# Kernel optimization log

Measured on AMD Instinct MI355X. Metric: run time of the kernel, lower is better.

The kernel has to match this reference:

```python
import jax, jax.numpy as jnp
import numpy as np

N, E, G = 50000, 600000, 512      # nodes, edges, graphs
FX, FE, H, OUT = 6, 4, 128, 1     # node feat, edge feat, hidden, output
T = 1.0                           # GENConv softmax temperature (learn_t=False default)
EPS = 1e-7                        # GENConv message eps


def setup_inputs() -> dict:
    key = jax.random.key(0)
    ks = jax.random.split(key, 12)
    return {
        "x": jax.random.normal(ks[0], (N, FX), jnp.float32),
        "edge_attr": jax.random.normal(ks[1], (E, FE), jnp.float32),
        "edge_index": jax.random.randint(ks[2], (2, E), 0, N),
        "batch": jnp.sort(jax.random.randint(ks[3], (N,), 0, G)),
        # node / edge encoders
        "wn": jax.random.normal(ks[4], (FX, H), jnp.float32) / np.sqrt(FX),
        "bn": jnp.zeros((H,), jnp.float32),
        "we": jax.random.normal(ks[5], (FE, H), jnp.float32) / np.sqrt(FE),
        "be": jnp.zeros((H,), jnp.float32),
        # 3 GENConv layers, params stacked on leading axis
        "cw1": jax.random.normal(ks[6], (3, H, 2 * H), jnp.float32) / np.sqrt(H),
        "cb1": jnp.zeros((3, 2 * H), jnp.float32),
        "cg": jnp.ones((3, 2 * H), jnp.float32),   # batchnorm gamma
        "cbt": jnp.zeros((3, 2 * H), jnp.float32), # batchnorm beta
        "cw2": jax.random.normal(ks[7], (3, 2 * H, H), jnp.float32) / np.sqrt(2 * H),
        "cb2": jnp.zeros((3, H), jnp.float32),
        # final dense
        "wd": jax.random.normal(ks[8], (H, OUT), jnp.float32) / np.sqrt(H),
        "bd": jnp.zeros((OUT,), jnp.float32),
    }


def _gen_conv(x, src, dst, edge_attr, w1, b1, g, bt, w2, b2):
    # message: relu(x_j + e_ij) + eps, aggregated with scatter-softmax over dst
    m = jax.nn.relu(x[src] + edge_attr) + EPS               # [E, H]
    z = m * T
    zmax = jax.lax.stop_gradient(jax.ops.segment_max(z, dst, num_segments=N))
    ez = jnp.exp(z - zmax[dst])
    denom = jax.ops.segment_sum(ez, dst, num_segments=N)
    alpha = ez / (denom[dst] + 1e-16)
    aggr = jax.ops.segment_sum(m * alpha, dst, num_segments=N)  # [N, H]
    h = aggr + x                                             # residual input to MLP
    # MLP: Linear(H,2H) -> BatchNorm(train mode) -> ReLU -> Linear(2H,H)
    h1 = h @ w1 + b1
    mu = h1.mean(0)
    var = h1.var(0)
    h1 = (h1 - mu) * jax.lax.rsqrt(var + 1e-5) * g + bt
    return jax.nn.relu(h1) @ w2 + b2


def reference(x, edge_attr, edge_index, batch, wn, bn, we, be,
              cw1, cb1, cg, cbt, cw2, cb2, wd, bd):
    src, dst = edge_index[0], edge_index[1]
    h = x @ wn + bn            # node encoder
    ea = edge_attr @ we + be   # edge encoder (shared across the 3 convs)
    for i in range(3):
        h = jax.nn.relu(_gen_conv(h, src, dst, ea,
                                  cw1[i], cb1[i], cg[i], cbt[i], cw2[i], cb2[i]))
    # global mean pool over graphs
    s = jax.ops.segment_sum(h, batch, num_segments=G)
    cnt = jax.ops.segment_sum(jnp.ones((N,), h.dtype), batch, num_segments=G)
    pooled = s / jnp.maximum(cnt, 1.0)[:, None]              # [G, H]
    return jax.nn.sigmoid(pooled @ wd + bd)                  # [G, OUT]
```

## Files before the change

kernel.cpp:

```cpp
#include <hip/hip_runtime.h>
#include <hip/hip_fp16.h>


#define HH 128
#define H2 256
#define MMP 256

typedef __attribute__((ext_vector_type(8))) short short8v;
typedef __attribute__((ext_vector_type(4))) float f32x4;
typedef __attribute__((ext_vector_type(2))) float f32x2;

__device__ __forceinline__ short f2bf(float f) {
  union { float f; unsigned u; } v; v.f = f;
  unsigned r = v.u + 0x7fff + ((v.u >> 16) & 1);
  return (short)(r >> 16);
}
__device__ __forceinline__ float bf2f(ushort s) {
  union { unsigned u; float f; } v; v.u = ((unsigned)s) << 16;
  return v.f;
}
__device__ __forceinline__ f32x2 splat2(float s) { return (f32x2){s, s}; }

__global__ void k_encode(const float* __restrict__ x, const float* __restrict__ wn,
                         const float* __restrict__ bnb, __half* __restrict__ h16, int n) {
  int c = threadIdx.x & 127;
  int node = blockIdx.x * 2 + (threadIdx.x >> 7);
  if (node >= n) return;
  const float* xr = x + (size_t)node * 6;
  float acc = bnb[c];
#pragma unroll
  for (int k = 0; k < 6; ++k) acc = fmaf(xr[k], wn[k * HH + c], acc);
  h16[(size_t)node * HH + c] = __float2half(acc);
}

__global__ void k_hist(const int* __restrict__ dst, int* __restrict__ counts,
                       const int* __restrict__ batch, float* __restrict__ cntf,
                       int E, int N) {
  int e = blockIdx.x * 256 + threadIdx.x;
  if (e < E) atomicAdd(&counts[dst[e]], 1);
  if (e < N) atomicAdd(&cntf[batch[e]], 1.f);
}

__global__ void k_scan(const int* __restrict__ counts, int* __restrict__ rowptr, int n) {
  __shared__ int wsum[16];
  __shared__ int carry;
  int t = threadIdx.x;
  int lane = t & 63, w = t >> 6;
  if (t == 0) carry = 0;
  __syncthreads();
  for (int base = 0; base < n; base += 4096) {
    int idx = base + t * 4;
    int4 v = make_int4(0, 0, 0, 0);
    if (idx + 3 < n) {
      v = *(const int4*)(counts + idx);
    } else {
      if (idx < n)     v.x = counts[idx];
      if (idx + 1 < n) v.y = counts[idx + 1];
      if (idx + 2 < n) v.z = counts[idx + 2];
    }
    int tsum = v.x + v.y + v.z + v.w;
    int x = tsum;
#pragma unroll
    for (int d = 1; d < 64; d <<= 1) {
      int y = __shfl_up(x, d);
      if (lane >= d) x += y;
    }
    if (lane == 63) wsum[w] = x;
    __syncthreads();
    if (w == 0 && lane < 16) {
      int s = wsum[lane];
#pragma unroll
      for (int d = 1; d < 16; d <<= 1) {
        int y = __shfl_up(s, d);
        if (lane >= d) s += y;
      }
      wsum[lane] = s;
    }
    __syncthreads();
    int waveoff = (w == 0) ? 0 : wsum[w - 1];
    int c0 = carry;
    int excl = c0 + waveoff + x - tsum;
    int4 o;
    o.x = excl;
    o.y = excl + v.x;
    o.z = o.y + v.y;
    o.w = o.z + v.z;
    if (idx + 3 < n) {
      *(int4*)(rowptr + idx) = o;
    } else {
      if (idx < n)     rowptr[idx] = o.x;
      if (idx + 1 < n) rowptr[idx + 1] = o.y;
      if (idx + 2 < n) rowptr[idx + 2] = o.z;
    }
    __syncthreads();
    if (t == 0) carry = c0 + wsum[15];
    __syncthreads();
  }
  if (t == 0) rowptr[n] = carry;
}

__global__ void k_fill(const int* __restrict__ src, const int* __restrict__ dst,
                       const float4* __restrict__ eattr,
                       const int* __restrict__ rowptr, int* __restrict__ fill,
                       int* __restrict__ ssrc, float4* __restrict__ eattrs, int E) {
  int e = blockIdx.x * 256 + threadIdx.x;
  if (e >= E) return;
  int d = dst[e];
  int pos = rowptr[d] + atomicAdd(&fill[d], 1);
  ssrc[pos] = src[e];
  eattrs[pos] = eattr[e];
}

__global__ __launch_bounds__(256) void k_conv(
    const __half* __restrict__ h16, const float4* __restrict__ eattrs,
    const float* __restrict__ we, const float* __restrict__ be,
    const int* __restrict__ rowptr, const int* __restrict__ ssrc,
    ushort* __restrict__ hresb, int n) {
  int d = blockIdx.x * 4 + (threadIdx.x >> 6);
  if (d >= n) return;
  int lane = threadIdx.x & 63;
  int c0 = lane * 2;
  f32x2 W0 = *(const f32x2*)(we + c0);
  f32x2 W1 = *(const f32x2*)(we + 128 + c0);
  f32x2 W2 = *(const f32x2*)(we + 256 + c0);
  f32x2 W3 = *(const f32x2*)(we + 384 + c0);
  f32x2 BE = *(const f32x2*)(be + c0);
  const f32x2 ZERO = splat2(0.f);
  const f32x2 EPS = splat2(1e-7f);
  int p0 = rowptr[d], p1 = rowptr[d + 1];
  f32x2 Sab = ZERO, Wab = ZERO, Scd = ZERO, Wcd = ZERO;
  int p = p0;
  for (; p + 4 <= p1; p += 4) {
    int sA = ssrc[p], sB = ssrc[p + 1], sC = ssrc[p + 2], sD = ssrc[p + 3];
    float4 aA = eattrs[p], aB = eattrs[p + 1], aC = eattrs[p + 2], aD = eattrs[p + 3];
    __half2 hA2 = *(const __half2*)(h16 + (size_t)sA * HH + c0);
    __half2 hB2 = *(const __half2*)(h16 + (size_t)sB * HH + c0);
    __half2 hC2 = *(const __half2*)(h16 + (size_t)sC * HH + c0);
    __half2 hD2 = *(const __half2*)(h16 + (size_t)sD * HH + c0);
    float2 hA = __half22float2(hA2), hB = __half22float2(hB2);
    float2 hC = __half22float2(hC2), hD = __half22float2(hD2);
    f32x2 eA = W0 * splat2(aA.x) + (W1 * splat2(aA.y) + (W2 * splat2(aA.z) + (W3 * splat2(aA.w) + BE)));
    f32x2 eB = W0 * splat2(aB.x) + (W1 * splat2(aB.y) + (W2 * splat2(aB.z) + (W3 * splat2(aB.w) + BE)));
    f32x2 eC = W0 * splat2(aC.x) + (W1 * splat2(aC.y) + (W2 * splat2(aC.z) + (W3 * splat2(aC.w) + BE)));
    f32x2 eD = W0 * splat2(aD.x) + (W1 * splat2(aD.y) + (W2 * splat2(aD.z) + (W3 * splat2(aD.w) + BE)));
    f32x2 mA = __builtin_elementwise_max((f32x2){hA.x, hA.y} + eA, ZERO) + EPS;
    f32x2 mB = __builtin_elementwise_max((f32x2){hB.x, hB.y} + eB, ZERO) + EPS;
    f32x2 mC = __builtin_elementwise_max((f32x2){hC.x, hC.y} + eC, ZERO) + EPS;
    f32x2 mD = __builtin_elementwise_max((f32x2){hD.x, hD.y} + eD, ZERO) + EPS;
    f32x2 xA = (f32x2){__expf(mA.x), __expf(mA.y)};
    f32x2 xB = (f32x2){__expf(mB.x), __expf(mB.y)};
    f32x2 xC = (f32x2){__expf(mC.x), __expf(mC.y)};
    f32x2 xD = (f32x2){__expf(mD.x), __expf(mD.y)};
    Sab += xA + xB;
    Scd += xC + xD;
    Wab += mA * xA + mB * xB;
    Wcd += mC * xC + mD * xD;
  }
  for (; p < p1; ++p) {
    int s = ssrc[p];
    float4 a = eattrs[p];
    __half2 hv2 = *(const __half2*)(h16 + (size_t)s * HH + c0);
    float2 hv = __half22float2(hv2);
    f32x2 e = W0 * splat2(a.x) + (W1 * splat2(a.y) + (W2 * splat2(a.z) + (W3 * splat2(a.w) + BE)));
    f32x2 m = __builtin_elementwise_max((f32x2){hv.x, hv.y} + e, ZERO) + EPS;
    f32x2 xe = (f32x2){__expf(m.x), __expf(m.y)};
    Sab += xe;
    Wab += m * xe;
  }
  f32x2 S = Sab + Scd, W = Wab + Wcd;
  __half2 hd2 = *(const __half2*)(h16 + (size_t)d * HH + c0);
  float2 hd = __half22float2(hd2);
  float r0 = W.x / (S.x + 1e-16f) + hd.x;
  float r1 = W.y / (S.y + 1e-16f) + hd.y;
  ushort2 o;
  o.x = (ushort)f2bf(r0);
  o.y = (ushort)f2bf(r1);
  *(ushort2*)(hresb + (size_t)d * HH + c0) = o;
}

__global__ void k_wconv(const float* __restrict__ W, short* __restrict__ out,
                        int logn, int K) {
  int layer = blockIdx.y;
  int total = K << logn;
  int e = blockIdx.x * 256 + threadIdx.x;
  if (e >= total) return;
  const float* Wl = W + (size_t)layer * total;
  short* ol = out + (size_t)layer * total;
  int k = e >> logn, col = e & ((1 << logn) - 1);
  int ty = col >> 7, colL = col & 127;
  int wc = colL >> 6, n = (colL >> 4) & 3, l15 = colL & 15;
  int kc = k >> 7, kl = k & 127;
  int ksl = kl >> 5, lhi = (kl >> 3) & 3, j = kl & 7;
  int KC = K >> 7;
  size_t idx = (size_t)(ty * KC + kc) * 16384 +
               ((((wc * 4 + n) * 4 + ksl) * 64 + lhi * 16 + l15) * 8 + j);
  ol[idx] = f2bf(Wl[e]);
}

__global__ __launch_bounds__(256) void k_mm1p(
    const ushort* __restrict__ Ab, const short* __restrict__ Bf,
    const float* __restrict__ bias, ushort* __restrict__ Cb,
    float* __restrict__ partial, int M, int mtiles) {
  __shared__ float red[256];
  int t = threadIdx.x;
  int bx = blockIdx.x, ty = blockIdx.y;
  int lane = t & 63, w = t >> 6;
  int wr = w >> 1, wc = w & 1;
  int l15 = lane & 15, lhi = lane >> 4;
  const short* Bt = Bf + (size_t)ty * 16384;
  short8v breg[4][4];
#pragma unroll
  for (int n = 0; n < 4; ++n)
#pragma unroll
    for (int ksl = 0; ksl < 4; ++ksl)
      breg[n][ksl] = *(const short8v*)(Bt + ((((wc * 4 + n) * 4 + ksl) * 64 + lane) * 8));
  float bb[4];
#pragma unroll
  for (int n = 0; n < 4; ++n) bb[n] = bias[ty * 128 + wc * 64 + n * 16 + l15];
  float cs[4] = {0.f, 0.f, 0.f, 0.f}, cq[4] = {0.f, 0.f, 0.f, 0.f};

  short8v a_cur[2][4], a_nxt[2][4];
  int tile = bx;
  if (tile < mtiles) {
    int row0 = tile * 64;
#pragma unroll
    for (int m = 0; m < 2; ++m) {
      int grow = row0 + (wr * 2 + m) * 16 + l15;
      if (grow < M) {
        const ushort* ap = Ab + (size_t)grow * HH + lhi * 8;
#pragma unroll
        for (int ksl = 0; ksl < 4; ++ksl) a_cur[m][ksl] = *(const short8v*)(ap + ksl * 32);
      } else {
#pragma unroll
        for (int ksl = 0; ksl < 4; ++ksl) a_cur[m][ksl] = (short8v){0,0,0,0,0,0,0,0};
      }
    }
  }
#pragma unroll 1
  for (; tile < mtiles; tile += MMP) {
    int nt = tile + MMP;
    if (nt < mtiles) {
      int row0n = nt * 64;
#pragma unroll
      for (int m = 0; m < 2; ++m) {
        int grow = row0n + (wr * 2 + m) * 16 + l15;
        if (grow < M) {
          const ushort* ap = Ab + (size_t)grow * HH + lhi * 8;
#pragma unroll
          for (int ksl = 0; ksl < 4; ++ksl) a_nxt[m][ksl] = *(const short8v*)(ap + ksl * 32);
        } else {
#pragma unroll
          for (int ksl = 0; ksl < 4; ++ksl) a_nxt[m][ksl] = (short8v){0,0,0,0,0,0,0,0};
        }
      }
    }
    f32x4 acc[2][4];
#pragma unroll
    for (int m = 0; m < 2; ++m)
#pragma unroll
      for (int n = 0; n < 4; ++n) acc[m][n] = (f32x4){0.f, 0.f, 0.f, 0.f};
#pragma unroll
    for (int ksl = 0; ksl < 4; ++ksl)
#pragma unroll
      for (int m = 0; m < 2; ++m)
#pragma unroll
        for (int n = 0; n < 4; ++n)
          acc[m][n] = __builtin_amdgcn_mfma_f32_16x16x32_bf16(a_cur[m][ksl], breg[n][ksl],
                                                              acc[m][n], 0, 0, 0);
    int row0 = tile * 64;
#pragma unroll
    for (int n = 0; n < 4; ++n) {
      int colL = wc * 64 + n * 16 + l15;
#pragma unroll
      for (int m = 0; m < 2; ++m) {
        int rbase = row0 + wr * 32 + m * 16 + lhi * 4;
#pragma unroll
        for (int r = 0; r < 4; ++r) {
          int row = rbase + r;
          if (row < M) {
            float o = acc[m][n][r] + bb[n];
            Cb[(size_t)row * H2 + ty * 128 + colL] = (ushort)f2bf(o);
            cs[n] += o; cq[n] += o * o;
          }
        }
      }
    }
#pragma unroll
    for (int m = 0; m < 2; ++m)
#pragma unroll
      for (int ksl = 0; ksl < 4; ++ksl) a_cur[m][ksl] = a_nxt[m][ksl];
  }
  red[t] = 0.f;
  __syncthreads();
#pragma unroll
  for (int n = 0; n < 4; ++n) {
    int colL = wc * 64 + n * 16 + l15;
    atomicAdd(&red[colL], cs[n]);
    atomicAdd(&red[128 + colL], cq[n]);
  }
  __syncthreads();
  partial[((size_t)(ty * MMP + bx)) * 256 + t] = red[t];
}

__global__ __launch_bounds__(1024) void k_bnfin(
    const float* __restrict__ partial, const float* __restrict__ g,
    const float* __restrict__ bt, float* __restrict__ scale,
    float* __restrict__ shift, float invN) {
  __shared__ float shs[1024], shq[1024];
  int t = threadIdx.x;
  int c = t & 255, seg = t >> 8;
  int ty = c >> 7, cl = c & 127;
  float s = 0.f, q = 0.f;
  const float* base = partial + (size_t)ty * MMP * 256;
#pragma unroll 8
  for (int bx = seg * 64; bx < seg * 64 + 64; ++bx) {
    s += base[(size_t)bx * 256 + cl];
    q += base[(size_t)bx * 256 + 128 + cl];
  }
  shs[t] = s; shq[t] = q;
  __syncthreads();
  if (t < 256) {
    s = shs[t] + shs[t + 256] + shs[t + 512] + shs[t + 768];
    q = shq[t] + shq[t + 256] + shq[t + 512] + shq[t + 768];
    float mu = s * invN;
    float var = q * invN - mu * mu;
    float rs = rsqrtf(var + 1e-5f);
    float sc = rs * g[t];
    scale[t] = sc;
    shift[t] = bt[t] - mu * sc;
  }
}

__global__ __launch_bounds__(256) void k_mm2f(
    const ushort* __restrict__ Ab, const short* __restrict__ Bf,
    const float* __restrict__ bias, const float* __restrict__ scale,
    const float* __restrict__ shift, __half* __restrict__ h16, int M) {
  int t = threadIdx.x;
  int row0 = blockIdx.x * 64;
  int lane = t & 63, w = t >> 6;
  int wr = w >> 1, wc = w & 1;
  int l15 = lane & 15, lhi = lane >> 4;
  int grow[2]; bool gv[2];
#pragma unroll
  for (int m = 0; m < 2; ++m) {
    grow[m] = row0 + (wr * 2 + m) * 16 + l15;
    gv[m] = grow[m] < M;
  }
  f32x4 acc[2][4];
#pragma unroll
  for (int m = 0; m < 2; ++m)
#pragma unroll
    for (int n = 0; n < 4; ++n) acc[m][n] = (f32x4){0.f, 0.f, 0.f, 0.f};
#pragma unroll 1
  for (int kc = 0; kc < 2; ++kc) {
    const short* Bk = Bf + (size_t)kc * 16384;
    short8v breg[4][4];
#pragma unroll
    for (int n = 0; n < 4; ++n)
#pragma unroll
      for (int ksl = 0; ksl < 4; ++ksl)
        breg[n][ksl] = *(const short8v*)(Bk + ((((wc * 4 + n) * 4 + ksl) * 64 + lane) * 8));
#pragma unroll
    for (int ksl = 0; ksl < 4; ++ksl) {
      int kb = kc * 128 + (ksl * 4 + lhi) * 8;
      float4 sc0 = *(const float4*)(scale + kb);
      float4 sc1 = *(const float4*)(scale + kb + 4);
      float4 sh0 = *(const float4*)(shift + kb);
      float4 sh1 = *(const float4*)(shift + kb + 4);
      short8v av[2];
#pragma unroll
      for (int m = 0; m < 2; ++m) {
        if (gv[m]) {
          short8v raw = *(const short8v*)(Ab + (size_t)grow[m] * H2 + kb);
          float f;
          f = fmaxf(fmaf(bf2f((ushort)raw[0]), sc0.x, sh0.x), 0.f); av[m][0] = f2bf(f);
          f = fmaxf(fmaf(bf2f((ushort)raw[1]), sc0.y, sh0.y), 0.f); av[m][1] = f2bf(f);
          f = fmaxf(fmaf(bf2f((ushort)raw[2]), sc0.z, sh0.z), 0.f); av[m][2] = f2bf(f);
          f = fmaxf(fmaf(bf2f((ushort)raw[3]), sc0.w, sh0.w), 0.f); av[m][3] = f2bf(f);
          f = fmaxf(fmaf(bf2f((ushort)raw[4]), sc1.x, sh1.x), 0.f); av[m][4] = f2bf(f);
          f = fmaxf(fmaf(bf2f((ushort)raw[5]), sc1.y, sh1.y), 0.f); av[m][5] = f2bf(f);
          f = fmaxf(fmaf(bf2f((ushort)raw[6]), sc1.z, sh1.z), 0.f); av[m][6] = f2bf(f);
          f = fmaxf(fmaf(bf2f((ushort)raw[7]), sc1.w, sh1.w), 0.f); av[m][7] = f2bf(f);
        } else {
          av[m] = (short8v){0,0,0,0,0,0,0,0};
        }
      }
#pragma unroll
      for (int m = 0; m < 2; ++m)
#pragma unroll
        for (int n = 0; n < 4; ++n)
          acc[m][n] = __builtin_amdgcn_mfma_f32_16x16x32_bf16(av[m], breg[n][ksl],
                                                              acc[m][n], 0, 0, 0);
    }
  }
#pragma unroll
  for (int n = 0; n < 4; ++n) {
    int colL = wc * 64 + n * 16 + l15;
    float bb = bias[colL];
#pragma unroll
    for (int m = 0; m < 2; ++m) {
      int rbase = row0 + wr * 32 + m * 16 + lhi * 4;
#pragma unroll
      for (int r = 0; r < 4; ++r) {
        int row = rbase + r;
        if (row < M)
          h16[(size_t)row * HH + colL] = __float2half(fmaxf(acc[m][n][r] + bb, 0.f));
      }
    }
  }
}

__global__ __launch_bounds__(128) void k_pool(const __half* __restrict__ h16,
                                              const int* __restrict__ batch,
                                              float* __restrict__ pool, int n) {
  int c = threadIdx.x;
  int n0 = blockIdx.x * 64;
  int nend = min(n0 + 64, n);
  float acc = 0.f;
  int gprev = batch[n0];
  for (int i = n0; i < nend; ++i) {
    int g = batch[i];
    if (g != gprev) {
      atomicAdd(&pool[(size_t)gprev * HH + c], acc);
      acc = 0.f;
      gprev = g;
    }
    acc += __half2float(h16[(size_t)i * HH + c]);
  }
  atomicAdd(&pool[(size_t)gprev * HH + c], acc);
}

__global__ __launch_bounds__(64) void k_final(const float* __restrict__ pool,
                                              const float* __restrict__ cntf,
                                              const float* __restrict__ wd,
                                              const float* __restrict__ bd,
                                              float* __restrict__ out) {
  int g = blockIdx.x;
  int t = threadIdx.x;
  float inv = 1.f / fmaxf(cntf[g], 1.f);
  float v = pool[(size_t)g * HH + t] * inv * wd[t] +
            pool[(size_t)g * HH + 64 + t] * inv * wd[64 + t];
#pragma unroll
  for (int d = 32; d; d >>= 1) v += __shfl_down(v, d);
  if (t == 0) out[g] = 1.f / (1.f + __expf(-(v + bd[0])));
}

extern "C" void kernel_launch(void* const* d_in, const int* in_sizes, int n_in,
                              void* d_out, int out_size, void* d_ws, size_t ws_size,
                              hipStream_t stream) {
  const float* x     = (const float*)d_in[0];
  const float* eattr = (const float*)d_in[1];
  const int*   eidx  = (const int*)d_in[2];
  const int*   batch = (const int*)d_in[3];
  const float* wn    = (const float*)d_in[4];
  const float* bnb   = (const float*)d_in[5];
  const float* we    = (const float*)d_in[6];
  const float* be    = (const float*)d_in[7];
  const float* cw1   = (const float*)d_in[8];
  const float* cb1   = (const float*)d_in[9];
  const float* cg    = (const float*)d_in[10];
  const float* cbt   = (const float*)d_in[11];
  const float* cw2   = (const float*)d_in[12];
  const float* cb2   = (const float*)d_in[13];
  const float* wd    = (const float*)d_in[14];
  const float* bd    = (const float*)d_in[15];
  float* out = (float*)d_out;

  const int N = in_sizes[0] / 6;
  const int E = in_sizes[1] / 4;
  const int G = out_size;

  const int* src = eidx;
  const int* dst = eidx + E;

  char* ws = (char*)d_ws;
  size_t off = 0;
  auto alloc = [&](size_t bytes) -> char* {
    char* p = ws + off;
    off = (off + bytes + 255) & ~(size_t)255;
    return p;
  };
  __half* h16     = (__half*)alloc((size_t)N * HH * 2);
  ushort* hresb   = (ushort*)alloc((size_t)N * HH * 2);
  ushort* h1b     = (ushort*)alloc((size_t)N * H2 * 2);
  int*    rowptr  = (int*)alloc((size_t)(N + 1) * 4);
  int*    counts  = (int*)alloc((size_t)N * 4);
  int*    fill    = (int*)alloc((size_t)N * 4);
  int*    ssrc    = (int*)alloc((size_t)E * 4);
  float4* eattrs  = (float4*)alloc((size_t)E * 16);
  float*  partial = (float*)alloc((size_t)2 * MMP * 256 * 4);
  float*  bnsc    = (float*)alloc(256 * 4);
  float*  bnsh    = (float*)alloc(256 * 4);
  float*  pool    = (float*)alloc((size_t)G * HH * 4);
  float*  cntf    = (float*)alloc((size_t)G * 4);
  short*  w1f     = (short*)alloc((size_t)3 * HH * H2 * 2);
  short*  w2f     = (short*)alloc((size_t)3 * H2 * HH * 2);

  (void)ws_size; (void)n_in;

  hipMemsetAsync(counts, 0, (size_t)N * 4, stream);
  hipMemsetAsync(fill, 0, (size_t)N * 4, stream);
  hipMemsetAsync(pool, 0, (size_t)G * HH * 4, stream);
  hipMemsetAsync(cntf, 0, (size_t)G * 4, stream);

  k_wconv<<<dim3(128, 3), 256, 0, stream>>>(cw1, w1f, 8, HH);
  k_wconv<<<dim3(128, 3), 256, 0, stream>>>(cw2, w2f, 7, H2);

  k_encode<<<(N + 1) / 2, 256, 0, stream>>>(x, wn, bnb, h16, N);
  k_hist<<<(E + 255) / 256, 256, 0, stream>>>(dst, counts, batch, cntf, E, N);
  k_scan<<<1, 1024, 0, stream>>>(counts, rowptr, N);
  k_fill<<<(E + 255) / 256, 256, 0, stream>>>(src, dst, (const float4*)eattr,
                                              rowptr, fill, ssrc, eattrs, E);

  int mtiles = (N + 63) / 64;
  for (int layer = 0; layer < 3; ++layer) {
    const short* w1 = w1f + (size_t)layer * HH * H2;
    const float* b1 = cb1 + (size_t)layer * H2;
    const float* g_ = cg + (size_t)layer * H2;
    const float* bt = cbt + (size_t)layer * H2;
    const short* w2 = w2f + (size_t)layer * H2 * HH;
    const float* b2 = cb2 + (size_t)layer * HH;

    k_conv<<<(N + 3) / 4, 256, 0, stream>>>(h16, eattrs, we, be, rowptr, ssrc, hresb, N);
    k_mm1p<<<dim3(MMP, 2), 256, 0, stream>>>(hresb, w1, b1, h1b, partial, N, mtiles);
    k_bnfin<<<1, 1024, 0, stream>>>(partial, g_, bt, bnsc, bnsh, 1.f / (float)N);
    k_mm2f<<<mtiles, 256, 0, stream>>>(h1b, w2, b2, bnsc, bnsh, h16, N);
  }

  k_pool<<<(N + 63) / 64, 128, 0, stream>>>(h16, batch, pool, N);
  k_final<<<G, 64, 0, stream>>>(pool, cntf, wd, bd, out);
}
```

Before: 559.8 us.

## Record atomic rank in histogram and count graph nodes via binary search

The histogram kernel now stores each edge's return value from its atomic increment as a rank, so the fill kernel computes its CSR position without a second round of atomics and the fill buffer and its memset go away. Per-graph node counts come from binary searches over the sorted batch array in a single-block kernel, replacing float atomics and a memset. This adds an E-sized rank buffer that is written and then read back, plus one extra small kernel launch. The binary-search count assumes batch is sorted.

```diff
diff --git a/kernel.cpp b/kernel.cpp
--- a/kernel.cpp
+++ b/kernel.cpp
@@ -34,11 +34,25 @@
 }
 
 __global__ void k_hist(const int* __restrict__ dst, int* __restrict__ counts,
-                       const int* __restrict__ batch, float* __restrict__ cntf,
-                       int E, int N) {
+                       int* __restrict__ rank, int E) {
   int e = blockIdx.x * 256 + threadIdx.x;
-  if (e < E) atomicAdd(&counts[dst[e]], 1);
-  if (e < N) atomicAdd(&cntf[batch[e]], 1.f);
+  if (e < E) rank[e] = atomicAdd(&counts[dst[e]], 1);
+}
+
+__global__ __launch_bounds__(1024) void k_cntg(const int* __restrict__ batch,
+                                               float* __restrict__ cntf, int n, int G) {
+  __shared__ int lb[513];
+  int t = threadIdx.x;
+  for (int v = t; v <= G; v += 1024) {
+    int lo = 0, hi = n;
+    while (lo < hi) {
+      int mid = (lo + hi) >> 1;
+      if (batch[mid] < v) lo = mid + 1; else hi = mid;
+    }
+    lb[v] = lo;
+  }
+  __syncthreads();
+  for (int g = t; g < G; g += 1024) cntf[g] = (float)(lb[g + 1] - lb[g]);
 }
 
 __global__ void k_scan(const int* __restrict__ counts, int* __restrict__ rowptr, int n) {
@@ -101,12 +115,11 @@
 
 __global__ void k_fill(const int* __restrict__ src, const int* __restrict__ dst,
                        const float4* __restrict__ eattr,
-                       const int* __restrict__ rowptr, int* __restrict__ fill,
+                       const int* __restrict__ rowptr, const int* __restrict__ rank,
                        int* __restrict__ ssrc, float4* __restrict__ eattrs, int E) {
   int e = blockIdx.x * 256 + threadIdx.x;
   if (e >= E) return;
-  int d = dst[e];
-  int pos = rowptr[d] + atomicAdd(&fill[d], 1);
+  int pos = rowptr[dst[e]] + rank[e];
   ssrc[pos] = src[e];
   eattrs[pos] = eattr[e];
 }
@@ -485,7 +498,7 @@
   ushort* h1b     = (ushort*)alloc((size_t)N * H2 * 2);
   int*    rowptr  = (int*)alloc((size_t)(N + 1) * 4);
   int*    counts  = (int*)alloc((size_t)N * 4);
-  int*    fill    = (int*)alloc((size_t)N * 4);
+  int*    rank    = (int*)alloc((size_t)E * 4);
   int*    ssrc    = (int*)alloc((size_t)E * 4);
   float4* eattrs  = (float4*)alloc((size_t)E * 16);
   float*  partial = (float*)alloc((size_t)2 * MMP * 256 * 4);
@@ -499,18 +512,17 @@
   (void)ws_size; (void)n_in;
 
   hipMemsetAsync(counts, 0, (size_t)N * 4, stream);
-  hipMemsetAsync(fill, 0, (size_t)N * 4, stream);
   hipMemsetAsync(pool, 0, (size_t)G * HH * 4, stream);
-  hipMemsetAsync(cntf, 0, (size_t)G * 4, stream);
 
   k_wconv<<<dim3(128, 3), 256, 0, stream>>>(cw1, w1f, 8, HH);
   k_wconv<<<dim3(128, 3), 256, 0, stream>>>(cw2, w2f, 7, H2);
 
   k_encode<<<(N + 1) / 2, 256, 0, stream>>>(x, wn, bnb, h16, N);
-  k_hist<<<(E + 255) / 256, 256, 0, stream>>>(dst, counts, batch, cntf, E, N);
+  k_hist<<<(E + 255) / 256, 256, 0, stream>>>(dst, counts, rank, E);
+  k_cntg<<<1, 1024, 0, stream>>>(batch, cntf, N, G);
   k_scan<<<1, 1024, 0, stream>>>(counts, rowptr, N);
   k_fill<<<(E + 255) / 256, 256, 0, stream>>>(src, dst, (const float4*)eattr,
-                                              rowptr, fill, ssrc, eattrs, E);
+                                              rowptr, rank, ssrc, eattrs, E);
 
   int mtiles = (N + 63) / 64;
   for (int layer = 0; layer < 3; ++layer) {
```

Result: faster. 497.3 us (-11.2%).
